# Optimization experiments

Hardware: AMD Instinct MI355X
Metric: run time of the kernel (lower is better)

The kernel has to match this reference:

```python
import jax, jax.numpy as jnp
import numpy as np
import math

EMBED_DIM = 768
NUM_HEADS = 12
HEAD_DIM = EMBED_DIM // NUM_HEADS
R = 16
LORA_ALPHA = 16
SCALING = LORA_ALPHA / math.sqrt(R)  # 4.0
U = 1.0  # ramp_up_steps=0 -> u()=1.0


def lora_linear(x, W, b, A):
    # base F.linear + SingLoRA delta: delta_W = A @ A.T (symmetric)
    base = x @ W.T + b
    delta_W = A @ A.T  # [D, D]
    return base + (x @ delta_W.T) * (U * SCALING)


def setup_inputs() -> dict:
    key = jax.random.key(0)
    ks = jax.random.split(key, 16)
    B, S, D = 2, 2048, EMBED_DIM
    inv = 1.0 / math.sqrt(D)
    d = {
        'query': jax.random.normal(ks[0], (B, S, D), jnp.float32),
        'key': jax.random.normal(ks[1], (B, S, D), jnp.float32),
        'value': jax.random.normal(ks[2], (B, S, D), jnp.float32),
        'Wq': jax.random.normal(ks[3], (D, D), jnp.float32) * inv,
        'bq': jax.random.normal(ks[4], (D,), jnp.float32) * 0.01,
        'Aq': jax.random.normal(ks[5], (D, R), jnp.float32) * 0.01,
        'Wk': jax.random.normal(ks[6], (D, D), jnp.float32) * inv,
        'bk': jax.random.normal(ks[7], (D,), jnp.float32) * 0.01,
        'Ak': jax.random.normal(ks[8], (D, R), jnp.float32) * 0.01,
        'Wv': jax.random.normal(ks[9], (D, D), jnp.float32) * inv,
        'bv': jax.random.normal(ks[10], (D,), jnp.float32) * 0.01,
        'Av': jax.random.normal(ks[11], (D, R), jnp.float32) * 0.01,
        'Wo': jax.random.normal(ks[12], (D, D), jnp.float32) * inv,
        'bo': jax.random.normal(ks[13], (D,), jnp.float32) * 0.01,
    }
    return d


def reference(query, key, value, Wq, bq, Aq, Wk, bk, Ak, Wv, bv, Av, Wo, bo):
    B, S, D = query.shape
    H, hd = NUM_HEADS, HEAD_DIM
    q = lora_linear(query, Wq, bq, Aq)
    k = lora_linear(key, Wk, bk, Ak)
    v = lora_linear(value, Wv, bv, Av)
    # [B, S, D] -> [B, H, S, hd]
    q = q.reshape(B, S, H, hd).transpose(0, 2, 1, 3)
    k = k.reshape(B, S, H, hd).transpose(0, 2, 1, 3)
    v = v.reshape(B, S, H, hd).transpose(0, 2, 1, 3)
    scores = jnp.einsum('bhqd,bhkd->bhqk', q, k) / math.sqrt(hd)
    attn = jax.nn.softmax(scores, axis=-1)
    out = jnp.einsum('bhqk,bhkd->bhqd', attn, v)  # [B, H, S, hd]
    out = out.transpose(0, 2, 1, 3).reshape(B, S, D)
    out = out @ Wo.T + bo
    return out
```

## Files before the change

### kernel.cpp

```cpp
#include <hip/hip_runtime.h>
#include <math.h>
#include <stdint.h>

#define D 768
#define S 2048
#define B_ 2
#define NROWS 4096
#define H 12
#define HD 64
#define R_ 16

typedef _Float16 half_t;
typedef _Float16 half8 __attribute__((ext_vector_type(8)));
typedef _Float16 half4 __attribute__((ext_vector_type(4)));
typedef float floatx4 __attribute__((ext_vector_type(4)));

#define MFMA32(a, b, c) __builtin_amdgcn_mfma_f32_16x16x32_f16(a, b, c, 0, 0, 0)
#define MFMA16(a, b, c) __builtin_amdgcn_mfma_f32_16x16x16f16(a, b, c, 0, 0, 0)
#define EXP2F(x) __builtin_amdgcn_exp2f(x)

__device__ __forceinline__ void gl_lds16(const void* gp, half_t* lp) {
  __builtin_amdgcn_global_load_lds(
      (const __attribute__((address_space(1))) void*)(gp),
      (__attribute__((address_space(3))) void*)(lp), 16, 0, 0);
}


__global__ __launch_bounds__(256) void prep_kernel(
    const float* __restrict__ q, const float* __restrict__ k,
    const float* __restrict__ v, half_t* __restrict__ xq,
    half_t* __restrict__ xk, half_t* __restrict__ xv,
    const float* __restrict__ Wq, const float* __restrict__ Aq,
    const float* __restrict__ Wk, const float* __restrict__ Ak,
    const float* __restrict__ Wv, const float* __restrict__ Av,
    const float* __restrict__ Wo, half_t* __restrict__ Mq,
    half_t* __restrict__ Mk, half_t* __restrict__ Mv,
    half_t* __restrict__ Mo) {
  const int bid = blockIdx.x;
  if (bid < 9216) {
    const int y = bid / 3072;
    const float* x = (y == 0) ? q : (y == 1) ? k : v;
    half_t* o = (y == 0) ? xq : (y == 1) ? xk : xv;
    int i = (bid - y * 3072) * 1024 + threadIdx.x * 4;
    float4 vv = *reinterpret_cast<const float4*>(x + i);
    half_t tmp[4] = {(half_t)vv.x, (half_t)vv.y, (half_t)vv.z, (half_t)vv.w};
    *reinterpret_cast<uint64_t*>(o + i) = *reinterpret_cast<uint64_t*>(tmp);
  } else {
    const int u = bid - 9216;
    const int y = u / 2304;
    const float* W = (y == 0) ? Wq : (y == 1) ? Wk : (y == 2) ? Wv : Wo;
    const float* A = (y == 0) ? Aq : (y == 1) ? Ak : (y == 2) ? Av : nullptr;
    half_t* M = (y == 0) ? Mq : (y == 1) ? Mk : (y == 2) ? Mv : Mo;
    int idx = (u - y * 2304) * 256 + threadIdx.x;
    int j = idx / D;
    int kk = idx - j * D;
    float acc = W[idx];
    if (A != nullptr) {
      float s = 0.f;
#pragma unroll
      for (int r = 0; r < R_; ++r) s += A[kk * R_ + r] * A[j * R_ + r];
      acc += 4.0f * s;
    }
    M[idx] = (half_t)acc;
  }
}

__global__ __launch_bounds__(256) void gemm_qkv_kernel(
    const half_t* __restrict__ x0, const half_t* __restrict__ x1,
    const half_t* __restrict__ x2, const half_t* __restrict__ m0,
    const half_t* __restrict__ m1, const half_t* __restrict__ m2,
    const float* __restrict__ b0, const float* __restrict__ b1,
    const float* __restrict__ b2, half_t* __restrict__ o0,
    half_t* __restrict__ o1, half_t* __restrict__ o2) {
  constexpr int AG = 8;
  constexpr int G = AG + 16;
  constexpr int PB = G * 512;
  __shared__ __align__(16) half_t smem[2 * PB];

  const int z = blockIdx.z;
  const half_t* X = (z == 0) ? x0 : (z == 1) ? x1 : x2;
  const half_t* M = (z == 0) ? m0 : (z == 1) ? m1 : m2;
  const float* bias = (z == 0) ? b0 : (z == 1) ? b1 : b2;
  half_t* Out = (z == 0) ? o0 : (z == 1) ? o1 : o2;

  const int tid = threadIdx.x;
  const int lane = tid & 63;
  const int wv = tid >> 6;
  const int lr = lane & 15;
  const int lq = lane >> 4;
  const int row0 = blockIdx.y * 64;
  const int j0 = blockIdx.x * 128;
  const int wc = wv;

  floatx4 acc[4][2] = {};

#define GSTAGE(bufi, k0)                                                       \
  do {                                                                         \
    _Pragma("unroll") for (int gi = 0; gi < 6; ++gi) {                         \
      int g = wv * 6 + gi;                                                     \
      if (g < AG) {                                                            \
        int t = g >> 1, c = g & 1;                                             \
        gl_lds16(                                                              \
            X + (size_t)(row0 + t * 16 + lr) * D + (k0) + c * 32 + lq * 8,     \
            smem + (bufi)*PB + g * 512);                                       \
      } else {                                                                 \
        int g2 = g - AG;                                                       \
        int u = g2 >> 1, c = g2 & 1;                                           \
        gl_lds16(                                                              \
            M + (size_t)(j0 + u * 16 + lr) * D + (k0) + c * 32 + lq * 8,       \
            smem + (bufi)*PB + AG * 512 + g2 * 512);                           \
      }                                                                        \
    }                                                                          \
  } while (0)

  GSTAGE(0, 0);
  __syncthreads();

  for (int it = 0; it < D / 64; ++it) {
    const int cur = it & 1;
    if (it + 1 < D / 64) GSTAGE(cur ^ 1, (it + 1) * 64);
    const half_t* Ab = smem + cur * PB;
    const half_t* Bb = Ab + AG * 512;
#pragma unroll
    for (int c = 0; c < 2; ++c) {
      half8 af[4], bf[2];
#pragma unroll
      for (int t = 0; t < 4; ++t)
        af[t] = *reinterpret_cast<const half8*>(
            &Ab[((t * 2 + c) * 64 + lane) * 8]);
#pragma unroll
      for (int u = 0; u < 2; ++u)
        bf[u] = *reinterpret_cast<const half8*>(
            &Bb[(((wc * 2 + u) * 2 + c) * 64 + lane) * 8]);
#pragma unroll
      for (int t = 0; t < 4; ++t)
#pragma unroll
        for (int u = 0; u < 2; ++u) acc[t][u] = MFMA32(af[t], bf[u], acc[t][u]);
    }
    __syncthreads();
  }
#undef GSTAGE

  float bv[2];
#pragma unroll
  for (int u = 0; u < 2; ++u) bv[u] = bias[j0 + (wc * 2 + u) * 16 + lr];

  if (z == 2) {
    const int bb = row0 >> 11;
    const int kb = (row0 & 2047) >> 6;
#pragma unroll
    for (int t = 0; t < 4; ++t) {
#pragma unroll
      for (int u = 0; u < 2; ++u) {
        int gc = j0 + (wc * 2 + u) * 16 + lr;
        int hh = gc >> 6;
        int ud = (wc * 2 + u) & 3;
        half4 hv;
#pragma unroll
        for (int r = 0; r < 4; ++r) hv[r] = (half_t)(acc[t][u][r] + bv[u]);
        size_t addr = ((size_t)(bb * H + hh) * HD) * S + (size_t)kb * 4096 +
                      (ud * 2 + (t >> 1)) * 512 + lane * 8 + (t & 1) * 4;
        *reinterpret_cast<half4*>(&Out[addr]) = hv;
      }
    }
    return;
  }

#pragma unroll
  for (int t = 0; t < 4; ++t) {
#pragma unroll
    for (int u = 0; u < 2; ++u) {
#pragma unroll
      for (int r = 0; r < 4; ++r) {
        int gr = row0 + t * 16 + lq * 4 + r;
        int gc = j0 + (wc * 2 + u) * 16 + lr;
        Out[(size_t)gr * D + gc] = (half_t)(acc[t][u][r] + bv[u]);
      }
    }
  }
}

__global__ __launch_bounds__(256) void gemm_o_kernel(
    const half_t* __restrict__ Xh, const half_t* __restrict__ M,
    const float* __restrict__ bias, float* __restrict__ Out) {
  constexpr int AG = 8;
  constexpr int G = 16;
  constexpr int PB = G * 512;
  __shared__ __align__(16) half_t smem[2 * PB];

  const int tid = threadIdx.x;
  const int lane = tid & 63;
  const int wv = tid >> 6;
  const int lr = lane & 15;
  const int lq = lane >> 4;
  const int row0 = blockIdx.y * 64;
  const int j0 = blockIdx.x * 64;
  const int wr = wv >> 1;
  const int wc = wv & 1;

  floatx4 acc[2][2] = {};

#define GSTAGE(bufi, k0)                                                       \
  do {                                                                         \
    _Pragma("unroll") for (int gi = 0; gi < 4; ++gi) {                         \
      int g = wv * 4 + gi;                                                     \
      if (g < AG) {                                                            \
        int t = g >> 1, c = g & 1;                                             \
        gl_lds16(                                                              \
            Xh + (size_t)(row0 + t * 16 + lr) * D + (k0) + c * 32 + lq * 8,    \
            smem + (bufi)*PB + g * 512);                                       \
      } else {                                                                 \
        int g2 = g - AG;                                                       \
        int u = g2 >> 1, c = g2 & 1;                                           \
        gl_lds16(                                                              \
            M + (size_t)(j0 + u * 16 + lr) * D + (k0) + c * 32 + lq * 8,       \
            smem + (bufi)*PB + AG * 512 + g2 * 512);                           \
      }                                                                        \
    }                                                                          \
  } while (0)

  GSTAGE(0, 0);
  __syncthreads();

  for (int it = 0; it < D / 64; ++it) {
    const int cur = it & 1;
    if (it + 1 < D / 64) GSTAGE(cur ^ 1, (it + 1) * 64);
    const half_t* Ab = smem + cur * PB;
    const half_t* Bb = Ab + AG * 512;
#pragma unroll
    for (int c = 0; c < 2; ++c) {
      half8 af[2], bf[2];
#pragma unroll
      for (int t = 0; t < 2; ++t)
        af[t] = *reinterpret_cast<const half8*>(
            &Ab[(((wr * 2 + t) * 2 + c) * 64 + lane) * 8]);
#pragma unroll
      for (int u = 0; u < 2; ++u)
        bf[u] = *reinterpret_cast<const half8*>(
            &Bb[(((wc * 2 + u) * 2 + c) * 64 + lane) * 8]);
#pragma unroll
      for (int t = 0; t < 2; ++t)
#pragma unroll
        for (int u = 0; u < 2; ++u) acc[t][u] = MFMA32(af[t], bf[u], acc[t][u]);
    }
    __syncthreads();
  }
#undef GSTAGE

  float bv[2];
#pragma unroll
  for (int u = 0; u < 2; ++u) bv[u] = bias[j0 + (wc * 2 + u) * 16 + lr];
#pragma unroll
  for (int t = 0; t < 2; ++t) {
#pragma unroll
    for (int u = 0; u < 2; ++u) {
#pragma unroll
      for (int r = 0; r < 4; ++r) {
        int gr = row0 + (wr * 2 + t) * 16 + lq * 4 + r;
        int gc = j0 + (wc * 2 + u) * 16 + lr;
        Out[(size_t)gr * D + gc] = acc[t][u][r] + bv[u];
      }
    }
  }
}

__global__ __launch_bounds__(512, 6) void attn_mfma_kernel(
    const half_t* __restrict__ Qh, const half_t* __restrict__ Kh,
    const half_t* __restrict__ Vt2, half_t* __restrict__ Oh) {
  __shared__ __align__(16) half_t smem[16384];
  half_t* Ks = smem;
  half_t* Vs = smem + 8192;

  const int tid = threadIdx.x;
  const int lane = tid & 63;
  const int wv = tid >> 6;
  const int t_ = wv & 3;
  const int half_ = wv >> 2;
  const int lr = lane & 15;
  const int lq = lane >> 4;
  const int q0 = blockIdx.x * 64;
  const int h = blockIdx.y;
  const int b = blockIdx.z;
  const size_t base = (size_t)b * S * D + h * HD;
  const size_t vtbase = (size_t)(b * H + h) * HD * (size_t)S;
  const int qw = q0 + t_ * 16;

  const half_t qscale = (half_t)0.18033688f;
  half8 qf[2];
#pragma unroll
  for (int c = 0; c < 2; ++c) {
    half8 qv = *reinterpret_cast<const half8*>(
        &Qh[base + (size_t)(qw + lr) * D + c * 32 + lq * 8]);
#pragma unroll
    for (int j = 0; j < 8; ++j) qv[j] = qv[j] * qscale;
    qf[c] = qv;
  }

  half4 ones;
#pragma unroll
  for (int j = 0; j < 4; ++j) ones[j] = (half_t)1.0f;

  floatx4 o[4] = {};
  floatx4 ol = {};

#define STAGE(bufi, kb)                                                        \
  do {                                                                         \
    _Pragma("unroll") for (int gi = 0; gi < 2; ++gi) {                         \
      int g = wv * 2 + gi;                                                     \
      if (g < 8) {                                                             \
        int u = g >> 1, c = g & 1;                                             \
        gl_lds16(                                                              \
            Kh + base + (size_t)((kb) + u * 16 + lr) * D + c * 32 + lq * 8,    \
            Ks + (bufi)*4096 + g * 512);                                       \
      } else {                                                                 \
        int gv = g - 8;                                                        \
        gl_lds16(Vt2 + vtbase + (size_t)(kb)*64 + gv * 512 + lane * 8,         \
                 Vs + (bufi)*4096 + gv * 512);                                 \
      }                                                                        \
    }                                                                          \
  } while (0)

  STAGE(0, 0);
  __syncthreads();

  for (int it = 0; it < S / 64; ++it) {
    const int cur = it & 1;
    if (it + 1 < S / 64) STAGE(cur ^ 1, (it + 1) * 64);

    half4 pf[2];
#pragma unroll
    for (int ui = 0; ui < 2; ++ui) {
      const int u = half_ * 2 + ui;
      half8 kf0 = *reinterpret_cast<const half8*>(
          &Ks[cur * 4096 + ((u * 2 + 0) * 64 + lane) * 8]);
      half8 kf1 = *reinterpret_cast<const half8*>(
          &Ks[cur * 4096 + ((u * 2 + 1) * 64 + lane) * 8]);
      floatx4 st = {};
      st = MFMA32(kf0, qf[0], st);
      st = MFMA32(kf1, qf[1], st);
      pf[ui][0] = (half_t)EXP2F(st[0]);
      pf[ui][1] = (half_t)EXP2F(st[1]);
      pf[ui][2] = (half_t)EXP2F(st[2]);
      pf[ui][3] = (half_t)EXP2F(st[3]);
    }
#pragma unroll
    for (int ud = 0; ud < 4; ++ud) {
      half8 vf8 = *reinterpret_cast<const half8*>(
          &Vs[cur * 4096 + ((ud * 2 + half_) * 64 + lane) * 8]);
      half4 vlo, vhi;
#pragma unroll
      for (int j = 0; j < 4; ++j) {
        vlo[j] = vf8[j];
        vhi[j] = vf8[4 + j];
      }
      o[ud] = MFMA16(pf[0], vlo, o[ud]);
      o[ud] = MFMA16(pf[1], vhi, o[ud]);
    }
    ol = MFMA16(pf[0], ones, ol);
    ol = MFMA16(pf[1], ones, ol);
    __syncthreads();
  }
#undef STAGE

  float* red = (float*)smem;
  const int slot = t_ * 64 + lane;
  if (half_ == 1) {
#pragma unroll
    for (int comp = 0; comp < 16; ++comp)
      red[comp * 260 + slot] = o[comp >> 2][comp & 3];
#pragma unroll
    for (int r = 0; r < 4; ++r) red[(16 + r) * 260 + slot] = ol[r];
  }
  __syncthreads();
  if (half_ == 0) {
#pragma unroll
    for (int comp = 0; comp < 16; ++comp)
      o[comp >> 2][comp & 3] += red[comp * 260 + slot];
    float linv[4];
#pragma unroll
    for (int r = 0; r < 4; ++r)
      linv[r] = 1.0f / (ol[r] + red[(16 + r) * 260 + slot]);
#pragma unroll
    for (int ud = 0; ud < 4; ++ud) {
#pragma unroll
      for (int r = 0; r < 4; ++r) {
        int row = qw + lq * 4 + r;
        int col = h * HD + ud * 16 + lr;
        Oh[(size_t)(b * S + row) * D + col] = (half_t)(o[ud][r] * linv[r]);
      }
    }
  }
}

extern "C" void kernel_launch(void* const* d_in, const int* in_sizes, int n_in,
                              void* d_out, int out_size, void* d_ws,
                              size_t ws_size, hipStream_t stream) {
  const float* query = (const float*)d_in[0];
  const float* key   = (const float*)d_in[1];
  const float* value = (const float*)d_in[2];
  const float* Wq = (const float*)d_in[3];
  const float* bq = (const float*)d_in[4];
  const float* Aq = (const float*)d_in[5];
  const float* Wk = (const float*)d_in[6];
  const float* bk = (const float*)d_in[7];
  const float* Ak = (const float*)d_in[8];
  const float* Wv = (const float*)d_in[9];
  const float* bv = (const float*)d_in[10];
  const float* Av = (const float*)d_in[11];
  const float* Wo = (const float*)d_in[12];
  const float* bo = (const float*)d_in[13];
  float* out = (float*)d_out;

  half_t* hw = (half_t*)d_ws;
  const size_t XSZ = (size_t)NROWS * D;
  const size_t MSZ = (size_t)D * D;
  half_t* xq = hw;
  half_t* xk = xq + XSZ;
  half_t* xv = xk + XSZ;
  half_t* qh = xv + XSZ;
  half_t* kh = qh + XSZ;
  half_t* vt = kh + XSZ;
  half_t* ab = vt + XSZ;
  half_t* Mq = ab + XSZ;
  half_t* Mk = Mq + MSZ;
  half_t* Mv = Mk + MSZ;
  half_t* Mo = Mv + MSZ;

  prep_kernel<<<18432, 256, 0, stream>>>(query, key, value, xq, xk, xv, Wq, Aq,
                                         Wk, Ak, Wv, Av, Wo, Mq, Mk, Mv, Mo);

  dim3 gq(D / 128, NROWS / 64, 3);
  gemm_qkv_kernel<<<gq, 256, 0, stream>>>(xq, xk, xv, Mq, Mk, Mv, bq, bk, bv,
                                          qh, kh, vt);

  dim3 ga(S / 64, H, B_);
  attn_mfma_kernel<<<ga, 512, 0, stream>>>(qh, kh, vt, ab);

  dim3 go(D / 64, NROWS / 64, 1);
  gemm_o_kernel<<<go, 256, 0, stream>>>(ab, Mo, bo, out);
}
```

Measured before the change: 223.1 us.

## Use triple-buffered LDS pipelines with partial vmcnt waits in GEMM and attention

Converts the double-buffered global-to-LDS staging in the QKV GEMM, output GEMM and attention kernels to a three-stage ring, prefetching two tiles ahead. The full __syncthreads is replaced by an explicit s_waitcnt that leaves the newest stage's loads in flight, followed by s_barrier, so memory latency overlaps more compute. LDS use per block grows by half, which can reduce occupancy. Correctness depends on the hand-encoded waitcnt immediates matching the number of loads each wave issues.

```diff
diff --git a/kernel.cpp b/kernel.cpp
--- a/kernel.cpp
+++ b/kernel.cpp
@@ -18,6 +18,9 @@
 #define MFMA32(a, b, c) __builtin_amdgcn_mfma_f32_16x16x32_f16(a, b, c, 0, 0, 0)
 #define MFMA16(a, b, c) __builtin_amdgcn_mfma_f32_16x16x16f16(a, b, c, 0, 0, 0)
 #define EXP2F(x) __builtin_amdgcn_exp2f(x)
+
+#define SWAIT(N) __builtin_amdgcn_s_waitcnt(0x0F70 | (N))
+#define SBAR() __builtin_amdgcn_s_barrier()
 
 __device__ __forceinline__ void gl_lds16(const void* gp, half_t* lp) {
   __builtin_amdgcn_global_load_lds(
@@ -75,7 +78,7 @@
   constexpr int AG = 8;
   constexpr int G = AG + 16;
   constexpr int PB = G * 512;
-  __shared__ __align__(16) half_t smem[2 * PB];
+  __shared__ __align__(16) half_t smem[3 * PB];
 
   const int z = blockIdx.z;
   const half_t* X = (z == 0) ? x0 : (z == 1) ? x1 : x2;
@@ -94,7 +97,7 @@
 
   floatx4 acc[4][2] = {};
 
-#define GSTAGE(bufi, k0)                                                       \
+#define GSTAGE(soff, k0)                                                       \
   do {                                                                         \
     _Pragma("unroll") for (int gi = 0; gi < 6; ++gi) {                         \
       int g = wv * 6 + gi;                                                     \
@@ -102,24 +105,26 @@
         int t = g >> 1, c = g & 1;                                             \
         gl_lds16(                                                              \
             X + (size_t)(row0 + t * 16 + lr) * D + (k0) + c * 32 + lq * 8,     \
-            smem + (bufi)*PB + g * 512);                                       \
+            smem + (soff) + g * 512);                                          \
       } else {                                                                 \
         int g2 = g - AG;                                                       \
         int u = g2 >> 1, c = g2 & 1;                                           \
         gl_lds16(                                                              \
             M + (size_t)(j0 + u * 16 + lr) * D + (k0) + c * 32 + lq * 8,       \
-            smem + (bufi)*PB + AG * 512 + g2 * 512);                           \
+            smem + (soff) + AG * 512 + g2 * 512);                              \
       }                                                                        \
     }                                                                          \
   } while (0)
 
   GSTAGE(0, 0);
-  __syncthreads();
-
+  GSTAGE(PB, 64);
+  SWAIT(6);
+  SBAR();
+
+  int co = 0, so = 2 * PB;
   for (int it = 0; it < D / 64; ++it) {
-    const int cur = it & 1;
-    if (it + 1 < D / 64) GSTAGE(cur ^ 1, (it + 1) * 64);
-    const half_t* Ab = smem + cur * PB;
+    if (it + 2 < D / 64) GSTAGE(so, (it + 2) * 64);
+    const half_t* Ab = smem + co;
     const half_t* Bb = Ab + AG * 512;
 #pragma unroll
     for (int c = 0; c < 2; ++c) {
@@ -137,7 +142,10 @@
 #pragma unroll
         for (int u = 0; u < 2; ++u) acc[t][u] = MFMA32(af[t], bf[u], acc[t][u]);
     }
-    __syncthreads();
+    if (it + 2 < D / 64) SWAIT(6); else SWAIT(0);
+    SBAR();
+    co += PB; if (co == 3 * PB) co = 0;
+    so += PB; if (so == 3 * PB) so = 0;
   }
 #undef GSTAGE
 
@@ -186,7 +194,7 @@
   constexpr int AG = 8;
   constexpr int G = 16;
   constexpr int PB = G * 512;
-  __shared__ __align__(16) half_t smem[2 * PB];
+  __shared__ __align__(16) half_t smem[3 * PB];
 
   const int tid = threadIdx.x;
   const int lane = tid & 63;
@@ -200,7 +208,7 @@
 
   floatx4 acc[2][2] = {};
 
-#define GSTAGE(bufi, k0)                                                       \
+#define GSTAGE(soff, k0)                                                       \
   do {                                                                         \
     _Pragma("unroll") for (int gi = 0; gi < 4; ++gi) {                         \
       int g = wv * 4 + gi;                                                     \
@@ -208,24 +216,26 @@
         int t = g >> 1, c = g & 1;                                             \
         gl_lds16(                                                              \
             Xh + (size_t)(row0 + t * 16 + lr) * D + (k0) + c * 32 + lq * 8,    \
-            smem + (bufi)*PB + g * 512);                                       \
+            smem + (soff) + g * 512);                                          \
       } else {                                                                 \
         int g2 = g - AG;                                                       \
         int u = g2 >> 1, c = g2 & 1;                                           \
         gl_lds16(                                                              \
             M + (size_t)(j0 + u * 16 + lr) * D + (k0) + c * 32 + lq * 8,       \
-            smem + (bufi)*PB + AG * 512 + g2 * 512);                           \
+            smem + (soff) + AG * 512 + g2 * 512);                              \
       }                                                                        \
     }                                                                          \
   } while (0)
 
   GSTAGE(0, 0);
-  __syncthreads();
-
+  GSTAGE(PB, 64);
+  SWAIT(4);
+  SBAR();
+
+  int co = 0, so = 2 * PB;
   for (int it = 0; it < D / 64; ++it) {
-    const int cur = it & 1;
-    if (it + 1 < D / 64) GSTAGE(cur ^ 1, (it + 1) * 64);
-    const half_t* Ab = smem + cur * PB;
+    if (it + 2 < D / 64) GSTAGE(so, (it + 2) * 64);
+    const half_t* Ab = smem + co;
     const half_t* Bb = Ab + AG * 512;
 #pragma unroll
     for (int c = 0; c < 2; ++c) {
@@ -243,7 +253,10 @@
 #pragma unroll
         for (int u = 0; u < 2; ++u) acc[t][u] = MFMA32(af[t], bf[u], acc[t][u]);
     }
-    __syncthreads();
+    if (it + 2 < D / 64) SWAIT(4); else SWAIT(0);
+    SBAR();
+    co += PB; if (co == 3 * PB) co = 0;
+    so += PB; if (so == 3 * PB) so = 0;
   }
 #undef GSTAGE
 
@@ -267,9 +280,9 @@
 __global__ __launch_bounds__(512, 6) void attn_mfma_kernel(
     const half_t* __restrict__ Qh, const half_t* __restrict__ Kh,
     const half_t* __restrict__ Vt2, half_t* __restrict__ Oh) {
-  __shared__ __align__(16) half_t smem[16384];
+  __shared__ __align__(16) half_t smem[24576];
   half_t* Ks = smem;
-  half_t* Vs = smem + 8192;
+  half_t* Vs = smem + 12288;
 
   const int tid = threadIdx.x;
   const int lane = tid & 63;
@@ -303,7 +316,7 @@
   floatx4 o[4] = {};
   floatx4 ol = {};
 
-#define STAGE(bufi, kb)                                                        \
+#define STAGE(soff, kb)                                                        \
   do {                                                                         \
     _Pragma("unroll") for (int gi = 0; gi < 2; ++gi) {                         \
       int g = wv * 2 + gi;                                                     \
@@ -311,30 +324,32 @@
         int u = g >> 1, c = g & 1;                                             \
         gl_lds16(                                                              \
             Kh + base + (size_t)((kb) + u * 16 + lr) * D + c * 32 + lq * 8,    \
-            Ks + (bufi)*4096 + g * 512);                                       \
+            Ks + (soff) + g * 512);                                            \
       } else {                                                                 \
         int gv = g - 8;                                                        \
         gl_lds16(Vt2 + vtbase + (size_t)(kb)*64 + gv * 512 + lane * 8,         \
-                 Vs + (bufi)*4096 + gv * 512);                                 \
+                 Vs + (soff) + gv * 512);                                      \
       }                                                                        \
     }                                                                          \
   } while (0)
 
   STAGE(0, 0);
-  __syncthreads();
-
+  STAGE(4096, 64);
+  SWAIT(2);
+  SBAR();
+
+  int co = 0, so = 8192;
   for (int it = 0; it < S / 64; ++it) {
-    const int cur = it & 1;
-    if (it + 1 < S / 64) STAGE(cur ^ 1, (it + 1) * 64);
+    if (it + 2 < S / 64) STAGE(so, (it + 2) * 64);
 
     half4 pf[2];
 #pragma unroll
     for (int ui = 0; ui < 2; ++ui) {
       const int u = half_ * 2 + ui;
       half8 kf0 = *reinterpret_cast<const half8*>(
-          &Ks[cur * 4096 + ((u * 2 + 0) * 64 + lane) * 8]);
+          &Ks[co + ((u * 2 + 0) * 64 + lane) * 8]);
       half8 kf1 = *reinterpret_cast<const half8*>(
-          &Ks[cur * 4096 + ((u * 2 + 1) * 64 + lane) * 8]);
+          &Ks[co + ((u * 2 + 1) * 64 + lane) * 8]);
       floatx4 st = {};
       st = MFMA32(kf0, qf[0], st);
       st = MFMA32(kf1, qf[1], st);
@@ -346,7 +361,7 @@
 #pragma unroll
     for (int ud = 0; ud < 4; ++ud) {
       half8 vf8 = *reinterpret_cast<const half8*>(
-          &Vs[cur * 4096 + ((ud * 2 + half_) * 64 + lane) * 8]);
+          &Vs[co + ((ud * 2 + half_) * 64 + lane) * 8]);
       half4 vlo, vhi;
 #pragma unroll
       for (int j = 0; j < 4; ++j) {
@@ -358,7 +373,11 @@
     }
     ol = MFMA16(pf[0], ones, ol);
     ol = MFMA16(pf[1], ones, ol);
-    __syncthreads();
+
+    if (it + 2 < S / 64) SWAIT(2); else SWAIT(0);
+    SBAR();
+    co += 4096; if (co == 12288) co = 0;
+    so += 4096; if (so == 12288) so = 0;
   }
 #undef STAGE
 
```

Measured after the change: 219.6 us. About the same (-1.6%).
